# Optimization experiments

Measured on AMD Instinct MI355X. Metric: run time of the kernel, lower is better.

Reference implementation:

```python
import jax, jax.numpy as jnp
import numpy as np

B = 131072
N_CAT = 29
VOCABS = np.array([2,2,2,2,2,3,3,4,4,4,3,3,3,4,4,4,4,4,4,4,2,2,2,2,2,2,2,2,2], dtype=np.int32)
MAX_V = 4
EPS = 1e-5


def setup_inputs():
    key = jax.random.key(0)
    ks = jax.random.split(key, 24)
    # input: [B, 36] = 7 continuous + 29 categorical (stored as float, cast in forward)
    xcon = jax.random.normal(ks[0], (B, 7), jnp.float32)
    raw = jax.random.randint(ks[1], (B, N_CAT), 0, 10_000)
    xcat = (raw % jnp.asarray(VOCABS)[None, :]).astype(jnp.float32)  # in-range per column
    x = jnp.concatenate([xcon, xcat], axis=1)
    s = 0.2
    # stacked per-feature branch params (embedding tables padded to MAX_V rows)
    E  = jax.random.normal(ks[2], (N_CAT, MAX_V, 12), jnp.float32)
    W1 = jax.random.normal(ks[3], (N_CAT, 12, 12), jnp.float32) * s
    b1 = jax.random.normal(ks[4], (N_CAT, 12), jnp.float32) * s
    W2 = jax.random.normal(ks[5], (N_CAT, 12), jnp.float32) * s
    b2 = jax.random.normal(ks[6], (N_CAT,), jnp.float32) * s
    rW1 = jax.random.normal(ks[7], (36, 768), jnp.float32) * s
    rb1 = jax.random.normal(ks[8], (768,), jnp.float32) * s
    g1  = jax.random.normal(ks[9], (768,), jnp.float32) * 0.1 + 1.0
    be1 = jax.random.normal(ks[10], (768,), jnp.float32) * 0.1
    m1  = jax.random.normal(ks[11], (768,), jnp.float32) * 0.1
    v1  = jnp.abs(jax.random.normal(ks[12], (768,), jnp.float32)) * 0.1 + 1.0
    rW2 = jax.random.normal(ks[13], (768, 64), jnp.float32) * (s / 4)
    rb2 = jax.random.normal(ks[14], (64,), jnp.float32) * s
    g2  = jax.random.normal(ks[15], (64,), jnp.float32) * 0.1 + 1.0
    be2 = jax.random.normal(ks[16], (64,), jnp.float32) * 0.1
    m2  = jax.random.normal(ks[17], (64,), jnp.float32) * 0.1
    v2  = jnp.abs(jax.random.normal(ks[18], (64,), jnp.float32)) * 0.1 + 1.0
    rW3 = jax.random.normal(ks[19], (64, 16), jnp.float32) * s
    rb3 = jax.random.normal(ks[20], (16,), jnp.float32) * s
    rW4 = jax.random.normal(ks[21], (16, 1), jnp.float32) * s
    rb4 = jax.random.normal(ks[22], (1,), jnp.float32) * s
    return dict(x=x, E=E, W1=W1, b1=b1, W2=W2, b2=b2,
                rW1=rW1, rb1=rb1, g1=g1, be1=be1, m1=m1, v1=v1,
                rW2=rW2, rb2=rb2, g2=g2, be2=be2, m2=m2, v2=v2,
                rW3=rW3, rb3=rb3, rW4=rW4, rb4=rb4)


def _forward(x, E, W1, b1, W2, b2, rW1, rb1, g1, be1, m1, v1,
             rW2, rb2, g2, be2, m2, v2, rW3, rb3, rW4, rb4):
    xcon = x[:, :7]
    idx = jax.lax.stop_gradient(x[:, 7:]).astype(jnp.int32)          # [B, 29]
    # batched gather: one embedding row per (sample, feature)
    emb = E[jnp.arange(N_CAT)[None, :], idx]                          # [B, 29, 12]
    h = jax.nn.relu(jnp.einsum('bfd,fde->bfe', emb, W1) + b1[None])   # [B, 29, 12]
    o = jax.nn.relu(jnp.einsum('bfd,fd->bf', h, W2) + b2[None])       # [B, 29]
    xin = jnp.concatenate([xcon, o], axis=1)                          # [B, 36]
    # head (BatchNorm eval mode, Dropout = identity)
    h1 = xin @ rW1 + rb1
    h1 = jax.nn.relu((h1 - m1) * jax.lax.rsqrt(v1 + EPS) * g1 + be1)
    h2 = h1 @ rW2 + rb2
    h2 = jax.nn.relu((h2 - m2) * jax.lax.rsqrt(v2 + EPS) * g2 + be2)
    h3 = jax.nn.relu(h2 @ rW3 + rb3)
    out = jax.nn.sigmoid(h3 @ rW4 + rb4)                              # [B, 1]
    return out


def reference(x, E, W1, b1, W2, b2, rW1, rb1, g1, be1, m1, v1,
              rW2, rb2, g2, be2, m2, v2, rW3, rb3, rW4, rb4):
    return _forward(x, E, W1, b1, W2, b2, rW1, rb1, g1, be1, m1, v1,
                    rW2, rb2, g2, be2, m2, v2, rW3, rb3, rW4, rb4)
```

## Files before the change

### kernel.cpp

```cpp
#include <hip/hip_runtime.h>
#include <math.h>

typedef _Float16 half8 __attribute__((ext_vector_type(8)));
typedef float floatx16 __attribute__((ext_vector_type(16)));
typedef unsigned int uintx4 __attribute__((ext_vector_type(4)));
typedef unsigned int uintx2 __attribute__((ext_vector_type(2)));

#define EPSV 1e-5f

#define CHUNK_BYTES 14336
#define OFF_TILES 0
#define OFF_W3    (12 * CHUNK_BYTES)
#define OFF_T2    (OFF_W3 + 4096)
#define OFF_OTAB  (OFF_T2 + 256)

__device__ __forceinline__ unsigned pk2(float a, float b) {
  _Float16 ha = (_Float16)a, hb = (_Float16)b;
  return (unsigned)__builtin_bit_cast(unsigned short, ha) |
         ((unsigned)__builtin_bit_cast(unsigned short, hb) << 16);
}
__device__ __forceinline__ void plswap(unsigned &a, unsigned &b) {
  uintx2 r = __builtin_amdgcn_permlane32_swap(a, b, false, false);
  a = r[0];
  b = r[1];
}
__device__ __forceinline__ half8 mk_bfrag(float v0, float v1, float v2, float v3,
                                          float v4, float v5, float v6, float v7) {
  unsigned r0 = pk2(fmaxf(v0, 0.f), fmaxf(v1, 0.f));
  unsigned r1 = pk2(fmaxf(v2, 0.f), fmaxf(v3, 0.f));
  unsigned r2 = pk2(fmaxf(v4, 0.f), fmaxf(v5, 0.f));
  unsigned r3 = pk2(fmaxf(v6, 0.f), fmaxf(v7, 0.f));
  plswap(r0, r2);
  plswap(r1, r3);
  uintx4 uv = {r0, r1, r2, r3};
  return __builtin_bit_cast(half8, uv);
}
__device__ __forceinline__ floatx16 zero16() {
  floatx16 z;
  #pragma unroll
  for (int i = 0; i < 16; ++i) z[i] = 0.f;
  return z;
}

__global__ void prep_kernel(const float* __restrict__ E,  const float* __restrict__ W1,
                            const float* __restrict__ b1, const float* __restrict__ W2,
                            const float* __restrict__ b2,
                            const float* __restrict__ rW1, const float* __restrict__ rb1,
                            const float* __restrict__ g1,  const float* __restrict__ be1,
                            const float* __restrict__ m1,  const float* __restrict__ v1,
                            const float* __restrict__ rW2, const float* __restrict__ rb2,
                            const float* __restrict__ g2,  const float* __restrict__ be2,
                            const float* __restrict__ m2,  const float* __restrict__ v2,
                            const float* __restrict__ rW3, char* __restrict__ ws)
{
  _Float16* tiles = (_Float16*)(ws + OFF_TILES);
  _Float16* w3t   = (_Float16*)(ws + OFF_W3);
  float*    t2o   = (float*)(ws + OFF_T2);
  float*    otab  = (float*)(ws + OFF_OTAB);

  const int NTI = 12 * 7168;
  const int NW3 = 2048;
  const int NT2 = 64;
  const int NOT = 116;
  const int NT  = NTI + NW3 + NT2 + NOT;

  for (int i = blockIdx.x * blockDim.x + threadIdx.x; i < NT; i += gridDim.x * blockDim.x) {
    int j = i;
    if (j < NTI) {
      const int ct = j / 7168;
      const int e  = j - ct * 7168;
      if (e < 3072) {
        const int f  = e >> 9, li = (e >> 3) & 63, el = e & 7;
        const int nt = f / 3, ks = f - nt * 3;
        const int n  = ct * 64 + nt * 32 + (li & 31);
        const int k  = ks * 16 + (li >> 5) * 8 + el;
        float val = 0.f;
        const float S1 = g1[n] * rsqrtf(v1[n] + EPSV);
        if (k < 36)       val = rW1[(size_t)k * 768 + n] * S1;
        else if (k == 36) val = (rb1[n] - m1[n]) * S1 + be1[n];
        tiles[j] = (_Float16)val;
      } else {
        const int e2 = e - 3072;
        const int f  = e2 >> 9, li = (e2 >> 3) & 63, el = e2 & 7;
        const int n2t = f >> 2, kc = f & 3;
        const int n2 = n2t * 32 + (li & 31);
        const int k  = ct * 64 + kc * 16 + (li >> 5) * 8 + el;
        const float S2 = g2[n2] * rsqrtf(v2[n2] + EPSV);
        tiles[j] = (_Float16)(rW2[(size_t)k * 64 + n2] * S2);
      }
      continue;
    }
    j -= NTI;
    if (j < NW3) {
      const int f3 = j >> 9, li = (j >> 3) & 63, el = j & 7;
      const int n3 = li & 31;
      const int k  = f3 * 16 + (li >> 5) * 8 + el;
      w3t[j] = (n3 < 16) ? (_Float16)rW3[(size_t)k * 16 + n3] : (_Float16)0.f;
      continue;
    }
    j -= NW3;
    if (j < NT2) {
      const float S2 = g2[j] * rsqrtf(v2[j] + EPSV);
      t2o[j] = (rb2[j] - m2[j]) * S2 + be2[j];
      continue;
    }
    j -= NT2;
    {
      const int f = j >> 2, v = j & 3;
      const float* ev  = E + ((f << 2) + v) * 12;
      const float* w1f = W1 + f * 144;
      float emb[12];
      #pragma unroll
      for (int d = 0; d < 12; ++d) emb[d] = ev[d];
      float acc_o = b2[f];
      #pragma unroll
      for (int ee = 0; ee < 12; ++ee) {
        float h = b1[f * 12 + ee];
        #pragma unroll
        for (int d = 0; d < 12; ++d) h = fmaf(emb[d], w1f[d * 12 + ee], h);
        h = fmaxf(h, 0.f);
        acc_o = fmaf(h, W2[f * 12 + ee], acc_o);
      }
      otab[f * 4 + v] = fmaxf(acc_o, 0.f);
    }
  }
}

__device__ __forceinline__ float feat_val(const float* xv, const float* otab, int c) {
  if (c < 7)  return xv[c];
  if (c < 36) return otab[(c - 7) * 4 + (int)xv[c]];
  if (c == 36) return 1.0f;
  return 0.f;
}

__global__ __launch_bounds__(256, 2)
void fused_mfma_kernel(const float* __restrict__ x,
                       const float* __restrict__ rb3,
                       const float* __restrict__ rW4,
                       const float* __restrict__ rb4,
                       const char* __restrict__ ws,
                       float* __restrict__ out)
{
  const int t  = threadIdx.x;
  const int w  = t >> 6;
  const int l  = t & 63;
  const int lm = l & 31;
  const int hi = l >> 5;

  const int nwg = gridDim.x;
  const int bid = (blockIdx.x & 7) * (nwg >> 3) + (blockIdx.x >> 3);
  const int b0 = bid * 256;

  unsigned wbits[24];
  {
    const float* xr = x + (size_t)(b0 + t) * 36;
    float xv[36];
    #pragma unroll
    for (int i = 0; i < 9; ++i) {
      float4 v = *(const float4*)(xr + 4 * i);
      xv[4 * i + 0] = v.x; xv[4 * i + 1] = v.y;
      xv[4 * i + 2] = v.z; xv[4 * i + 3] = v.w;
    }
    const float* otab = (const float*)(ws + OFF_OTAB);
    #pragma unroll
    for (int c2 = 0; c2 < 19; ++c2)
      wbits[c2] = pk2(feat_val(xv, otab, 2 * c2), feat_val(xv, otab, 2 * c2 + 1));
    #pragma unroll
    for (int c2 = 19; c2 < 24; ++c2) wbits[c2] = 0u;
  }

  half8 xf[2][3];
  #pragma unroll
  for (int ks = 0; ks < 3; ++ks) {
    unsigned w0[4], w1[4];
    #pragma unroll
    for (int q = 0; q < 4; ++q) {
      unsigned a = wbits[ks * 8 + q];
      unsigned b = wbits[ks * 8 + 4 + q];
      plswap(a, b);
      w0[q] = a; w1[q] = b;
    }
    uintx4 u0 = {w0[0], w0[1], w0[2], w0[3]};
    uintx4 u1 = {w1[0], w1[1], w1[2], w1[3]};
    xf[0][ks] = __builtin_bit_cast(half8, u0);
    xf[1][ks] = __builtin_bit_cast(half8, u1);
  }

  const char* wsl = ws + (size_t)l * 16;

  floatx16 acc00 = zero16(), acc01 = zero16(), acc10 = zero16(), acc11 = zero16();

  #pragma unroll
  for (int ct = 0; ct < 12; ++ct) {
    const char* src = wsl + (size_t)ct * CHUNK_BYTES;
    half8 w1c[6], w2c[8];
    #pragma unroll
    for (int f = 0; f < 6; ++f)
      w1c[f] = *(const half8*)(src + f * 1024);
    #pragma unroll
    for (int f = 0; f < 8; ++f)
      w2c[f] = *(const half8*)(src + 6144 + f * 1024);

    __builtin_amdgcn_s_setprio(1);
    floatx16 p0m0 = zero16(), p0m1 = zero16();
    floatx16 p1m0 = zero16(), p1m1 = zero16();
    #pragma unroll
    for (int ks = 0; ks < 3; ++ks) {
      p0m0 = __builtin_amdgcn_mfma_f32_32x32x16_f16(w1c[ks],     xf[0][ks], p0m0, 0, 0, 0);
      p0m1 = __builtin_amdgcn_mfma_f32_32x32x16_f16(w1c[ks],     xf[1][ks], p0m1, 0, 0, 0);
      p1m0 = __builtin_amdgcn_mfma_f32_32x32x16_f16(w1c[3 + ks], xf[0][ks], p1m0, 0, 0, 0);
      p1m1 = __builtin_amdgcn_mfma_f32_32x32x16_f16(w1c[3 + ks], xf[1][ks], p1m1, 0, 0, 0);
    }
    #pragma unroll
    for (int nt = 0; nt < 2; ++nt) {
      const floatx16 c1m0 = nt ? p1m0 : p0m0;
      const floatx16 c1m1 = nt ? p1m1 : p0m1;
      #pragma unroll
      for (int hf = 0; hf < 2; ++hf) {
        const int kc = nt * 2 + hf;
        const int b = hf * 8;
        half8 bf0 = mk_bfrag(c1m0[b+0], c1m0[b+1], c1m0[b+2], c1m0[b+3],
                             c1m0[b+4], c1m0[b+5], c1m0[b+6], c1m0[b+7]);
        half8 bf1 = mk_bfrag(c1m1[b+0], c1m1[b+1], c1m1[b+2], c1m1[b+3],
                             c1m1[b+4], c1m1[b+5], c1m1[b+6], c1m1[b+7]);
        acc00 = __builtin_amdgcn_mfma_f32_32x32x16_f16(w2c[0 * 4 + kc], bf0, acc00, 0, 0, 0);
        acc01 = __builtin_amdgcn_mfma_f32_32x32x16_f16(w2c[0 * 4 + kc], bf1, acc01, 0, 0, 0);
        acc10 = __builtin_amdgcn_mfma_f32_32x32x16_f16(w2c[1 * 4 + kc], bf0, acc10, 0, 0, 0);
        acc11 = __builtin_amdgcn_mfma_f32_32x32x16_f16(w2c[1 * 4 + kc], bf1, acc11, 0, 0, 0);
      }
    }
    __builtin_amdgcn_s_setprio(0);
  }

  const float* T2p = (const float*)(ws + OFF_T2);
  const _Float16* gW3 = (const _Float16*)(ws + OFF_W3);
  floatx16 c3a = zero16(), c3b = zero16();

  #pragma unroll
  for (int n2t = 0; n2t < 2; ++n2t) {
    float t2v[16];
    #pragma unroll
    for (int r = 0; r < 16; ++r)
      t2v[r] = T2p[n2t * 32 + (r & 3) + 8 * (r >> 2) + 4 * hi];
    const floatx16 am0 = n2t ? acc10 : acc00;
    const floatx16 am1 = n2t ? acc11 : acc01;
    float h0[16], h1v[16];
    #pragma unroll
    for (int r = 0; r < 16; ++r) {
      h0[r]  = fmaxf(am0[r] + t2v[r], 0.f);
      h1v[r] = fmaxf(am1[r] + t2v[r], 0.f);
    }
    #pragma unroll
    for (int hf = 0; hf < 2; ++hf) {
      const int kc = n2t * 2 + hf;
      const int b = hf * 8;
      half8 bf0 = mk_bfrag(h0[b+0], h0[b+1], h0[b+2], h0[b+3], h0[b+4], h0[b+5], h0[b+6], h0[b+7]);
      half8 bf1 = mk_bfrag(h1v[b+0], h1v[b+1], h1v[b+2], h1v[b+3], h1v[b+4], h1v[b+5], h1v[b+6], h1v[b+7]);
      half8 a3 = *(const half8*)&gW3[(kc * 64 + l) * 8];
      c3a = __builtin_amdgcn_mfma_f32_32x32x16_f16(a3, bf0, c3a, 0, 0, 0);
      c3b = __builtin_amdgcn_mfma_f32_32x32x16_f16(a3, bf1, c3b, 0, 0, 0);
    }
  }
  {
    float rb3v[8], rw4v[8];
    #pragma unroll
    for (int r = 0; r < 8; ++r) {
      const int n3 = (r & 3) + 8 * (r >> 2) + 4 * hi;
      rb3v[r] = rb3[n3];
      rw4v[r] = rW4[n3];
    }
    const float bb = rb4[0];
    float s0 = 0.f, s1 = 0.f;
    #pragma unroll
    for (int r = 0; r < 8; ++r) {
      s0 += fmaxf(c3a[r] + rb3v[r], 0.f) * rw4v[r];
      s1 += fmaxf(c3b[r] + rb3v[r], 0.f) * rw4v[r];
    }
    s0 += __shfl_xor(s0, 32, 64);
    s1 += __shfl_xor(s1, 32, 64);
    if (hi == 0) {
      out[b0 + (2 * w + 0) * 32 + lm] = 1.f / (1.f + expf(-(s0 + bb)));
      out[b0 + (2 * w + 1) * 32 + lm] = 1.f / (1.f + expf(-(s1 + bb)));
    }
  }
}

extern "C" void kernel_launch(void* const* d_in, const int* in_sizes, int n_in,
                              void* d_out, int out_size, void* d_ws, size_t ws_size,
                              hipStream_t stream) {
  const float* x   = (const float*)d_in[0];
  const float* E   = (const float*)d_in[1];
  const float* W1  = (const float*)d_in[2];
  const float* b1  = (const float*)d_in[3];
  const float* W2  = (const float*)d_in[4];
  const float* b2  = (const float*)d_in[5];
  const float* rW1 = (const float*)d_in[6];
  const float* rb1 = (const float*)d_in[7];
  const float* g1  = (const float*)d_in[8];
  const float* be1 = (const float*)d_in[9];
  const float* m1  = (const float*)d_in[10];
  const float* v1  = (const float*)d_in[11];
  const float* rW2 = (const float*)d_in[12];
  const float* rb2 = (const float*)d_in[13];
  const float* g2  = (const float*)d_in[14];
  const float* be2 = (const float*)d_in[15];
  const float* m2  = (const float*)d_in[16];
  const float* v2  = (const float*)d_in[17];
  const float* rW3 = (const float*)d_in[18];
  const float* rb3 = (const float*)d_in[19];
  const float* rW4 = (const float*)d_in[20];
  const float* rb4 = (const float*)d_in[21];
  float* out = (float*)d_out;
  char* ws = (char*)d_ws;

  prep_kernel<<<128, 256, 0, stream>>>(E, W1, b1, W2, b2,
                                       rW1, rb1, g1, be1, m1, v1,
                                       rW2, rb2, g2, be2, m2, v2,
                                       rW3, ws);

  const int B = in_sizes[0] / 36;
  dim3 grid(B / 256), block(256);
  fused_mfma_kernel<<<grid, block, 0, stream>>>(x, rb3, rW4, rb4, ws, out);
}
```

Baseline: 33.08 us.

## Halve rows per wave to cut register pressure and raise occupancy

```diff
diff --git a/kernel.cpp b/kernel.cpp
--- a/kernel.cpp
+++ b/kernel.cpp
@@ -133,7 +133,7 @@
   return 0.f;
 }
 
-__global__ __launch_bounds__(256, 2)
+__global__ __launch_bounds__(256, 3)
 void fused_mfma_kernel(const float* __restrict__ x,
                        const float* __restrict__ rb3,
                        const float* __restrict__ rW4,
@@ -149,11 +149,12 @@
 
   const int nwg = gridDim.x;
   const int bid = (blockIdx.x & 7) * (nwg >> 3) + (blockIdx.x >> 3);
-  const int b0 = bid * 256;
+  const int b0 = bid * 128;
+  const int row = b0 + w * 32 + lm;
 
   unsigned wbits[24];
   {
-    const float* xr = x + (size_t)(b0 + t) * 36;
+    const float* xr = x + (size_t)row * 36;
     float xv[36];
     #pragma unroll
     for (int i = 0; i < 9; ++i) {
@@ -169,26 +170,20 @@
     for (int c2 = 19; c2 < 24; ++c2) wbits[c2] = 0u;
   }
 
-  half8 xf[2][3];
+  half8 xf[3];
   #pragma unroll
   for (int ks = 0; ks < 3; ++ks) {
-    unsigned w0[4], w1[4];
-    #pragma unroll
-    for (int q = 0; q < 4; ++q) {
-      unsigned a = wbits[ks * 8 + q];
-      unsigned b = wbits[ks * 8 + 4 + q];
-      plswap(a, b);
-      w0[q] = a; w1[q] = b;
-    }
-    uintx4 u0 = {w0[0], w0[1], w0[2], w0[3]};
-    uintx4 u1 = {w1[0], w1[1], w1[2], w1[3]};
-    xf[0][ks] = __builtin_bit_cast(half8, u0);
-    xf[1][ks] = __builtin_bit_cast(half8, u1);
+    unsigned wq[4];
+    #pragma unroll
+    for (int q = 0; q < 4; ++q)
+      wq[q] = hi ? wbits[ks * 8 + 4 + q] : wbits[ks * 8 + q];
+    uintx4 u = {wq[0], wq[1], wq[2], wq[3]};
+    xf[ks] = __builtin_bit_cast(half8, u);
   }
 
   const char* wsl = ws + (size_t)l * 16;
 
-  floatx16 acc00 = zero16(), acc01 = zero16(), acc10 = zero16(), acc11 = zero16();
+  floatx16 acc0 = zero16(), acc1 = zero16();
 
   #pragma unroll
   for (int ct = 0; ct < 12; ++ct) {
@@ -202,31 +197,20 @@
       w2c[f] = *(const half8*)(src + 6144 + f * 1024);
 
     __builtin_amdgcn_s_setprio(1);
-    floatx16 p0m0 = zero16(), p0m1 = zero16();
-    floatx16 p1m0 = zero16(), p1m1 = zero16();
-    #pragma unroll
-    for (int ks = 0; ks < 3; ++ks) {
-      p0m0 = __builtin_amdgcn_mfma_f32_32x32x16_f16(w1c[ks],     xf[0][ks], p0m0, 0, 0, 0);
-      p0m1 = __builtin_amdgcn_mfma_f32_32x32x16_f16(w1c[ks],     xf[1][ks], p0m1, 0, 0, 0);
-      p1m0 = __builtin_amdgcn_mfma_f32_32x32x16_f16(w1c[3 + ks], xf[0][ks], p1m0, 0, 0, 0);
-      p1m1 = __builtin_amdgcn_mfma_f32_32x32x16_f16(w1c[3 + ks], xf[1][ks], p1m1, 0, 0, 0);
-    }
     #pragma unroll
     for (int nt = 0; nt < 2; ++nt) {
-      const floatx16 c1m0 = nt ? p1m0 : p0m0;
-      const floatx16 c1m1 = nt ? p1m1 : p0m1;
+      floatx16 c1m = zero16();
+      #pragma unroll
+      for (int ks = 0; ks < 3; ++ks)
+        c1m = __builtin_amdgcn_mfma_f32_32x32x16_f16(w1c[nt * 3 + ks], xf[ks], c1m, 0, 0, 0);
       #pragma unroll
       for (int hf = 0; hf < 2; ++hf) {
         const int kc = nt * 2 + hf;
         const int b = hf * 8;
-        half8 bf0 = mk_bfrag(c1m0[b+0], c1m0[b+1], c1m0[b+2], c1m0[b+3],
-                             c1m0[b+4], c1m0[b+5], c1m0[b+6], c1m0[b+7]);
-        half8 bf1 = mk_bfrag(c1m1[b+0], c1m1[b+1], c1m1[b+2], c1m1[b+3],
-                             c1m1[b+4], c1m1[b+5], c1m1[b+6], c1m1[b+7]);
-        acc00 = __builtin_amdgcn_mfma_f32_32x32x16_f16(w2c[0 * 4 + kc], bf0, acc00, 0, 0, 0);
-        acc01 = __builtin_amdgcn_mfma_f32_32x32x16_f16(w2c[0 * 4 + kc], bf1, acc01, 0, 0, 0);
-        acc10 = __builtin_amdgcn_mfma_f32_32x32x16_f16(w2c[1 * 4 + kc], bf0, acc10, 0, 0, 0);
-        acc11 = __builtin_amdgcn_mfma_f32_32x32x16_f16(w2c[1 * 4 + kc], bf1, acc11, 0, 0, 0);
+        half8 bf = mk_bfrag(c1m[b+0], c1m[b+1], c1m[b+2], c1m[b+3],
+                            c1m[b+4], c1m[b+5], c1m[b+6], c1m[b+7]);
+        acc0 = __builtin_amdgcn_mfma_f32_32x32x16_f16(w2c[0 * 4 + kc], bf, acc0, 0, 0, 0);
+        acc1 = __builtin_amdgcn_mfma_f32_32x32x16_f16(w2c[1 * 4 + kc], bf, acc1, 0, 0, 0);
       }
     }
     __builtin_amdgcn_s_setprio(0);
@@ -234,54 +218,38 @@
 
   const float* T2p = (const float*)(ws + OFF_T2);
   const _Float16* gW3 = (const _Float16*)(ws + OFF_W3);
-  floatx16 c3a = zero16(), c3b = zero16();
+  floatx16 c3 = zero16();
 
   #pragma unroll
   for (int n2t = 0; n2t < 2; ++n2t) {
-    float t2v[16];
-    #pragma unroll
-    for (int r = 0; r < 16; ++r)
-      t2v[r] = T2p[n2t * 32 + (r & 3) + 8 * (r >> 2) + 4 * hi];
-    const floatx16 am0 = n2t ? acc10 : acc00;
-    const floatx16 am1 = n2t ? acc11 : acc01;
-    float h0[16], h1v[16];
+    const floatx16 am = n2t ? acc1 : acc0;
+    float h0[16];
     #pragma unroll
     for (int r = 0; r < 16; ++r) {
-      h0[r]  = fmaxf(am0[r] + t2v[r], 0.f);
-      h1v[r] = fmaxf(am1[r] + t2v[r], 0.f);
+      const float t2v = T2p[n2t * 32 + (r & 3) + 8 * (r >> 2) + 4 * hi];
+      h0[r] = fmaxf(am[r] + t2v, 0.f);
     }
     #pragma unroll
     for (int hf = 0; hf < 2; ++hf) {
       const int kc = n2t * 2 + hf;
       const int b = hf * 8;
-      half8 bf0 = mk_bfrag(h0[b+0], h0[b+1], h0[b+2], h0[b+3], h0[b+4], h0[b+5], h0[b+6], h0[b+7]);
-      half8 bf1 = mk_bfrag(h1v[b+0], h1v[b+1], h1v[b+2], h1v[b+3], h1v[b+4], h1v[b+5], h1v[b+6], h1v[b+7]);
+      half8 bf = mk_bfrag(h0[b+0], h0[b+1], h0[b+2], h0[b+3],
+                          h0[b+4], h0[b+5], h0[b+6], h0[b+7]);
       half8 a3 = *(const half8*)&gW3[(kc * 64 + l) * 8];
-      c3a = __builtin_amdgcn_mfma_f32_32x32x16_f16(a3, bf0, c3a, 0, 0, 0);
-      c3b = __builtin_amdgcn_mfma_f32_32x32x16_f16(a3, bf1, c3b, 0, 0, 0);
+      c3 = __builtin_amdgcn_mfma_f32_32x32x16_f16(a3, bf, c3, 0, 0, 0);
     }
   }
   {
-    float rb3v[8], rw4v[8];
+    float s0 = 0.f;
+    const float bb = rb4[0];
     #pragma unroll
     for (int r = 0; r < 8; ++r) {
       const int n3 = (r & 3) + 8 * (r >> 2) + 4 * hi;
-      rb3v[r] = rb3[n3];
-      rw4v[r] = rW4[n3];
-    }
-    const float bb = rb4[0];
-    float s0 = 0.f, s1 = 0.f;
-    #pragma unroll
-    for (int r = 0; r < 8; ++r) {
-      s0 += fmaxf(c3a[r] + rb3v[r], 0.f) * rw4v[r];
-      s1 += fmaxf(c3b[r] + rb3v[r], 0.f) * rw4v[r];
+      s0 += fmaxf(c3[r] + rb3[n3], 0.f) * rW4[n3];
     }
     s0 += __shfl_xor(s0, 32, 64);
-    s1 += __shfl_xor(s1, 32, 64);
-    if (hi == 0) {
-      out[b0 + (2 * w + 0) * 32 + lm] = 1.f / (1.f + expf(-(s0 + bb)));
-      out[b0 + (2 * w + 1) * 32 + lm] = 1.f / (1.f + expf(-(s1 + bb)));
-    }
+    if (hi == 0)
+      out[row] = 1.f / (1.f + expf(-(s0 + bb)));
   }
 }
 
@@ -319,6 +287,6 @@
                                        rW3, ws);
 
   const int B = in_sizes[0] / 36;
-  dim3 grid(B / 256), block(256);
+  dim3 grid(B / 128), block(256);
   fused_mfma_kernel<<<grid, block, 0, stream>>>(x, rb3, rW4, rb4, ws, out);
 }
```

After: 40.04 us. 21.0% more time.

## Stage weight chunks through double-buffered LDS with async global-to-LDS loads

Applied to the files above, without the earlier changes.

```diff
diff --git a/kernel.cpp b/kernel.cpp
--- a/kernel.cpp
+++ b/kernel.cpp
@@ -13,6 +13,9 @@
 #define OFF_W3    (12 * CHUNK_BYTES)
 #define OFF_T2    (OFF_W3 + 4096)
 #define OFF_OTAB  (OFF_T2 + 256)
+
+typedef __attribute__((address_space(3))) char      lds_char;
+typedef __attribute__((address_space(3))) unsigned  lds_uint;
 
 __device__ __forceinline__ unsigned pk2(float a, float b) {
   _Float16 ha = (_Float16)a, hb = (_Float16)b;
@@ -133,6 +136,19 @@
   return 0.f;
 }
 
+__device__ __forceinline__ void stage_chunk(const char* gsrc, lds_char* ldst, int w, int l) {
+  #pragma unroll
+  for (int i = 0; i < 4; ++i) {
+    const int f = w + 4 * i;
+    if (f < 14) {
+      __builtin_amdgcn_global_load_lds(
+          (const __attribute__((address_space(1))) unsigned int*)(gsrc + f * 1024 + (size_t)l * 16),
+          (lds_uint*)(ldst + f * 1024),
+          16, 0, 0);
+    }
+  }
+}
+
 __global__ __launch_bounds__(256, 2)
 void fused_mfma_kernel(const float* __restrict__ x,
                        const float* __restrict__ rb3,
@@ -151,6 +167,13 @@
   const int bid = (blockIdx.x & 7) * (nwg >> 3) + (blockIdx.x >> 3);
   const int b0 = bid * 256;
 
+  __shared__ __align__(16) char smem[2 * CHUNK_BYTES];
+  lds_char* lds0 = (lds_char*)smem;
+
+  const char* tiles = ws + OFF_TILES;
+
+  stage_chunk(tiles, lds0, w, l);
+
   unsigned wbits[24];
   {
     const float* xr = x + (size_t)(b0 + t) * 36;
@@ -186,20 +209,26 @@
     xf[1][ks] = __builtin_bit_cast(half8, u1);
   }
 
-  const char* wsl = ws + (size_t)l * 16;
+  __syncthreads();
 
   floatx16 acc00 = zero16(), acc01 = zero16(), acc10 = zero16(), acc11 = zero16();
 
   #pragma unroll
   for (int ct = 0; ct < 12; ++ct) {
-    const char* src = wsl + (size_t)ct * CHUNK_BYTES;
+    const char* cbuf = smem + (ct & 1) * CHUNK_BYTES;
+
+    if (ct < 11)
+      stage_chunk(tiles + (size_t)(ct + 1) * CHUNK_BYTES,
+                  lds0 + ((ct + 1) & 1) * CHUNK_BYTES, w, l);
+
+    const char* srcl = cbuf + (size_t)l * 16;
     half8 w1c[6], w2c[8];
     #pragma unroll
     for (int f = 0; f < 6; ++f)
-      w1c[f] = *(const half8*)(src + f * 1024);
+      w1c[f] = *(const half8*)(srcl + f * 1024);
     #pragma unroll
     for (int f = 0; f < 8; ++f)
-      w2c[f] = *(const half8*)(src + 6144 + f * 1024);
+      w2c[f] = *(const half8*)(srcl + 6144 + f * 1024);
 
     __builtin_amdgcn_s_setprio(1);
     floatx16 p0m0 = zero16(), p0m1 = zero16();
@@ -230,6 +259,9 @@
       }
     }
     __builtin_amdgcn_s_setprio(0);
+
+    if (ct < 11)
+      __syncthreads();
   }
 
   const float* T2p = (const float*)(ws + OFF_T2);
```

Measured after the change: 33.14 us. About the same (+0.2%).
